# Kernel tuning notes

Measured on AMD Instinct MI355X. Metric: run time of the kernel, lower is better.

Reference implementation:

```python
import jax, jax.numpy as jnp
import numpy as np

TEMP = 0.1
EPS = 1e-08

def _l2norm(x):
    # F.normalize semantics: x / max(||x||, 1e-12)
    n = jnp.linalg.norm(x, axis=-1, keepdims=True)
    return x / jnp.maximum(n, 1e-12)

def setup_inputs() -> dict:
    key = jax.random.key(0)
    k0, k1, k2, k3, k4 = jax.random.split(key, 5)
    B, Ph, Pw, D, O = 32, 32, 32, 512, 128
    P = Ph * Pw
    patch_features = jax.random.normal(k0, (B, Ph, Pw, D), jnp.float32)
    obj_features = jax.random.normal(k1, (B, O, D), jnp.float32)
    # e1i: each patch positively matched to one object (one-hot rows)
    idx = jax.random.randint(k2, (B, P), 0, O)
    e1i = jax.nn.one_hot(idx, O, dtype=jnp.float32)
    # e1j / e2j: sparse binary negative masks
    e1j = (jax.random.uniform(k3, (B, P, P)) < 0.1).astype(jnp.float32)
    e2j = (jax.random.uniform(k4, (B, P, O)) < 0.1).astype(jnp.float32)
    return {"patch_features": patch_features, "obj_features": obj_features,
            "e1i": e1i, "e1j": e1j, "e2j": e2j}

def reference(patch_features, obj_features, e1i, e1j, e2j):
    B, D = patch_features.shape[0], patch_features.shape[-1]
    pf = patch_features.reshape(B, -1, D)          # [B, P, D]
    pn = _l2norm(pf)
    on = _l2norm(obj_features)                     # [B, O, D]
    po_sim = jnp.einsum('bpd,bod->bpo', pn, on)    # patch-object cosine sim
    po_exp = jnp.exp(po_sim / TEMP)
    pp_exp = jnp.exp(jnp.einsum('bpd,bqd->bpq', pn, pn) / TEMP)
    delta_E1i_E2i = jnp.sum(e1i * po_exp, axis=-1)     # [B, P]
    sum_E1i_E1j = jnp.sum(e1j * pp_exp, axis=-1)
    sum_E1i_E2j = jnp.sum(e2j * po_exp, axis=-1)
    ratio = delta_E1i_E2i / (delta_E1i_E2i + sum_E1i_E1j + sum_E1i_E2j + EPS)
    loss_all = -jnp.log(ratio + EPS)                   # [B, P]
    valid = (jnp.sum(e1i, axis=-1) > 0).astype(loss_all.dtype)  # [B, P]
    n_valid = jnp.sum(valid)
    loss = jnp.sum(loss_all * valid) / n_valid
    matched = jnp.argmax(po_sim, axis=-1)              # [B, P]
    labels = jnp.take_along_axis(e1i, matched[..., None], axis=-1)[..., 0]
    matched_success_ratio = jnp.sum(labels * valid) / n_valid
    return loss, matched_success_ratio
```

## Files before the change

kernel.cpp:

```cpp
#include <hip/hip_runtime.h>
#include <hip/hip_bf16.h>

constexpr int BB = 32;
constexpr int P  = 1024;
constexpr int O  = 128;
constexpr int D  = 512;
constexpr float EPS = 1e-8f;
constexpr float SCL = 14.426950408889634f;

typedef __attribute__((ext_vector_type(8))) short short8;
typedef __attribute__((ext_vector_type(16))) float f32x16;

__device__ __forceinline__ unsigned short f2bf(float f) {
  __hip_bfloat16 h = __float2bfloat16(f);
  unsigned short u;
  __builtin_memcpy(&u, &h, sizeof(u));
  return u;
}

__device__ __forceinline__ void gld_lds16(const void* g, void* l) {
  __builtin_amdgcn_global_load_lds(
      (const __attribute__((address_space(1))) void*)g,
      (__attribute__((address_space(3))) void*)l, 16, 0, 0);
}

__global__ __launch_bounds__(256) void prep_kernel(
    const float* __restrict__ pf, const float* __restrict__ of,
    __hip_bfloat16* __restrict__ pn, __hip_bfloat16* __restrict__ on) {
  int lane = threadIdx.x & 63;
  int row = blockIdx.x * 4 + (threadIdx.x >> 6);
  const float* src;
  __hip_bfloat16* dst;
  if (row < BB * P) {
    src = pf + (size_t)row * D;
    dst = pn + (size_t)row * D;
  } else {
    int r = row - BB * P;
    if (r >= BB * O) return;
    src = of + (size_t)r * D;
    dst = on + (size_t)r * D;
  }
  float4 v0 = *(const float4*)(src + lane * 8);
  float4 v1 = *(const float4*)(src + lane * 8 + 4);
  float ss = v0.x * v0.x + v0.y * v0.y + v0.z * v0.z + v0.w * v0.w +
             v1.x * v1.x + v1.y * v1.y + v1.z * v1.z + v1.w * v1.w;
  #pragma unroll
  for (int s = 1; s < 64; s <<= 1) ss += __shfl_xor(ss, s);
  float sc = 1.0f / fmaxf(sqrtf(ss), 1e-12f);
  short8 w;
  w[0] = (short)f2bf(v0.x * sc); w[1] = (short)f2bf(v0.y * sc);
  w[2] = (short)f2bf(v0.z * sc); w[3] = (short)f2bf(v0.w * sc);
  w[4] = (short)f2bf(v1.x * sc); w[5] = (short)f2bf(v1.y * sc);
  w[6] = (short)f2bf(v1.z * sc); w[7] = (short)f2bf(v1.w * sc);
  *reinterpret_cast<short8*>(dst + lane * 8) = w;
}

__global__ __launch_bounds__(256, 3) void icl_main7(
    const __hip_bfloat16* __restrict__ pn, const __hip_bfloat16* __restrict__ on,
    const float* __restrict__ e1i, const float* __restrict__ e1j,
    const float* __restrict__ e2j,
    float* __restrict__ d_row, float* __restrict__ s1_row,
    float* __restrict__ s2_row, unsigned long long* __restrict__ pk_row,
    int* __restrict__ ip_row) {

  __shared__ __hip_bfloat16 As[128 * 64];
  __shared__ __hip_bfloat16 Bs[128 * 64];

  const int tid  = threadIdx.x;
  const int l    = tid & 63;
  const int wid  = tid >> 6;
  const int wr   = wid >> 1;
  const int wc   = wid & 1;
  const int half = l >> 5;
  const int l31  = l & 31;

  const int bid   = blockIdx.x;
  const int batch = bid & 31;
  const int unit  = bid >> 5;
  const int rt    = unit & 7;
  const int ct    = unit >> 3;
  const int row0  = rt * 128;

  const __hip_bfloat16* pnb = pn + (size_t)batch * P * D;
  const __hip_bfloat16* onb = on + (size_t)batch * O * D;
  const __hip_bfloat16* asrc = pnb + (size_t)row0 * D;
  const __hip_bfloat16* bsrc = (ct == 0) ? onb : pnb + (size_t)(ct - 1) * 128 * D;

  auto stage = [&](const __hip_bfloat16* __restrict__ src,
                   __hip_bfloat16* __restrict__ lds, int k0) {
    #pragma unroll
    for (int i = 0; i < 4; ++i) {
      int q = i * 256 + tid;
      int rr = q >> 3, c = q & 7;
      int gc = c ^ (rr & 7);
      gld_lds16(src + (size_t)rr * D + k0 + (gc << 3),
                (char*)lds + (size_t)(i * 256 + wid * 64) * 16);
    }
  };

  f32x16 acc[2][2];
  #pragma unroll
  for (int m = 0; m < 2; ++m)
    #pragma unroll
    for (int n = 0; n < 2; ++n)
      #pragma unroll
      for (int k = 0; k < 16; ++k) acc[m][n][k] = 0.f;

  for (int ks = 0; ks < 8; ++ks) {
    __syncthreads();
    stage(asrc, As, ks * 64);
    stage(bsrc, Bs, ks * 64);
    __syncthreads();
    #pragma unroll
    for (int kc = 0; kc < 4; ++kc) {
      const int ch = (kc << 1) | half;
      short8 af[2], bfr[2];
      #pragma unroll
      for (int m = 0; m < 2; ++m) {
        int row = wr * 64 + m * 32 + l31;
        af[m] = *reinterpret_cast<const short8*>(
            As + row * 64 + ((ch ^ (row & 7)) << 3));
      }
      #pragma unroll
      for (int n = 0; n < 2; ++n) {
        int col = wc * 64 + n * 32 + l31;
        bfr[n] = *reinterpret_cast<const short8*>(
            Bs + col * 64 + ((ch ^ (col & 7)) << 3));
      }
      #pragma unroll
      for (int m = 0; m < 2; ++m)
        #pragma unroll
        for (int n = 0; n < 2; ++n)
          acc[m][n] = __builtin_amdgcn_mfma_f32_32x32x16_bf16(
              af[m], bfr[n], acc[m][n], 0, 0, 0);
    }
  }

  if (ct == 0) {
    #pragma unroll
    for (int m = 0; m < 2; ++m) {
      #pragma unroll
      for (int r = 0; r < 16; ++r) {
        const int lrow = wr * 64 + m * 32 + (r & 3) + ((r >> 2) << 3) + (half << 2);
        const size_t grow = (size_t)batch * P + row0 + lrow;
        const size_t gb = grow * O;
        const int c0 = wc * 64 + l31, c1 = wc * 64 + 32 + l31;
        float s0 = acc[m][0][r], s1v = acc[m][1][r];
        float e0 = exp2f(s0 * SCL), e1 = exp2f(s1v * SCL);
        float m10 = e1i[gb + c0], m11 = e1i[gb + c1];
        float m20 = e2j[gb + c0], m21 = e2j[gb + c1];
        float dv  = m10 * e0 + m11 * e1;
        float s2v = m20 * e0 + m21 * e1;
        int ipv = (m11 > 0.5f) ? c1 : ((m10 > 0.5f) ? c0 : -1);
        float mvv; int miv;
        if (s1v > s0) { mvv = s1v; miv = c1; } else { mvv = s0; miv = c0; }
        #pragma unroll
        for (int s = 1; s < 32; s <<= 1) {
          dv  += __shfl_xor(dv, s);
          s2v += __shfl_xor(s2v, s);
          ipv  = max(ipv, __shfl_xor(ipv, s));
          float ov = __shfl_xor(mvv, s);
          int   oi = __shfl_xor(miv, s);
          if (ov > mvv || (ov == mvv && oi < miv)) { mvv = ov; miv = oi; }
        }
        if (l31 == 0) {
          if (dv != 0.f) atomicAdd(&d_row[grow], dv);
          atomicAdd(&s2_row[grow], s2v);
          unsigned long long pkv =
              ((unsigned long long)__float_as_uint(mvv + 2.0f) << 32) |
              (unsigned)(0xFFFFFFFFu - (unsigned)miv);
          atomicMax(&pk_row[grow], pkv);
          if (ipv >= 0) atomicMax(&ip_row[grow], ipv);
        }
      }
    }
  } else {
    const int pb = (ct - 1) * 128;
    #pragma unroll
    for (int m = 0; m < 2; ++m) {
      #pragma unroll
      for (int r = 0; r < 16; ++r) {
        const int lrow = wr * 64 + m * 32 + (r & 3) + ((r >> 2) << 3) + (half << 2);
        const size_t grow = (size_t)batch * P + row0 + lrow;
        const size_t gb = grow * P + pb;
        const int c0 = wc * 64 + l31, c1 = wc * 64 + 32 + l31;
        float v = e1j[gb + c0] * exp2f(acc[m][0][r] * SCL) +
                  e1j[gb + c1] * exp2f(acc[m][1][r] * SCL);
        #pragma unroll
        for (int s = 1; s < 32; s <<= 1) v += __shfl_xor(v, s);
        if (l31 == 0) atomicAdd(&s1_row[grow], v);
      }
    }
  }
}

__global__ __launch_bounds__(256) void icl_reduce(
    const float* __restrict__ d_row, const float* __restrict__ s1_row,
    const float* __restrict__ s2_row, const unsigned long long* __restrict__ pk_row,
    const int* __restrict__ ip_row, float* __restrict__ accum) {
  __shared__ float red[12];
  const int tid = threadIdx.x;
  const int row = blockIdx.x * 256 + tid;
  float d = d_row[row], a = s1_row[row], c = s2_row[row];
  int ipv = ip_row[row];
  int miv = (int)(0xFFFFFFFFu - (unsigned)(pk_row[row] & 0xFFFFFFFFull));
  float valid = (ipv >= 0) ? 1.f : 0.f;
  float ratio = d / (d + a + c + EPS);
  float lsum = -logf(ratio + EPS) * valid;
  float lbl  = (ipv >= 0 && miv == ipv) ? 1.f : 0.f;
  float vct  = valid;
  #pragma unroll
  for (int s = 1; s < 64; s <<= 1) {
    lsum += __shfl_xor(lsum, s);
    lbl  += __shfl_xor(lbl, s);
    vct  += __shfl_xor(vct, s);
  }
  const int wid = tid >> 6;
  if ((tid & 63) == 0) {
    red[wid * 3 + 0] = lsum;
    red[wid * 3 + 1] = lbl;
    red[wid * 3 + 2] = vct;
  }
  __syncthreads();
  if (tid == 0) {
    atomicAdd(&accum[0], red[0] + red[3] + red[6] + red[9]);
    atomicAdd(&accum[1], red[1] + red[4] + red[7] + red[10]);
    atomicAdd(&accum[2], red[2] + red[5] + red[8] + red[11]);
  }
}

__global__ void finalize_kernel(const float* __restrict__ accum,
                                float* __restrict__ out) {
  if (threadIdx.x == 0 && blockIdx.x == 0) {
    float nv = accum[2];
    out[0] = accum[0] / nv;
    out[1] = accum[1] / nv;
  }
}

__global__ __launch_bounds__(256) void norm_kernel(
    const float* __restrict__ pf, const float* __restrict__ of,
    float* __restrict__ invp, float* __restrict__ invo) {
  int lane = threadIdx.x & 63;
  int row = blockIdx.x * 4 + (threadIdx.x >> 6);
  const float* src;
  float* dst;
  if (row < BB * P) {
    src = pf + (size_t)row * D;
    dst = invp + row;
  } else {
    int r = row - BB * P;
    if (r >= BB * O) return;
    src = of + (size_t)r * D;
    dst = invo + r;
  }
  float ss = 0.f;
  #pragma unroll
  for (int i = 0; i < 2; ++i) {
    float4 v = *(const float4*)(src + (lane + 64 * i) * 4);
    ss += v.x * v.x + v.y * v.y + v.z * v.z + v.w * v.w;
  }
  #pragma unroll
  for (int s = 1; s < 64; s <<= 1) ss += __shfl_xor(ss, s);
  if (lane == 0) *dst = 1.0f / fmaxf(sqrtf(ss), 1e-12f);
}

__global__ __launch_bounds__(256) void icl_main_v1(
    const float* __restrict__ pf, const float* __restrict__ of,
    const float* __restrict__ e1i, const float* __restrict__ e1j,
    const float* __restrict__ e2j, const float* __restrict__ invp,
    const float* __restrict__ invo, float* __restrict__ accum) {
  constexpr int PT = 128, BK = 64;
  __shared__ __hip_bfloat16 As[PT * BK];
  __shared__ __hip_bfloat16 Bs[PT * BK];
  __shared__ float d_l[2][PT], s2_l[2][PT], ei_l[2][PT], s1_l[2][PT], mv_l[2][PT];
  __shared__ int   mi_l[2][PT];
  __shared__ float red[12];

  const int tid  = threadIdx.x;
  const int lane = tid & 63;
  const int wid  = tid >> 6;
  const int wr   = wid >> 1;
  const int wc   = wid & 1;
  const int half = lane >> 5;
  const int l31  = lane & 31;
  const int b    = blockIdx.x & 31;
  const int pt   = blockIdx.x >> 5;
  const int row0 = pt * PT;

  const float* pfb = pf + (size_t)b * P * D;
  const float* ofb = of + (size_t)b * O * D;
  const float* ivp = invp + b * P + row0;
  const float* ivq = invp + b * P;
  const float* ivo = invo + b * O;

  float s1p[2][16];
  #pragma unroll
  for (int m = 0; m < 2; ++m)
    #pragma unroll
    for (int r = 0; r < 16; ++r) s1p[m][r] = 0.f;

  auto stage = [&](const float* __restrict__ src, const float* __restrict__ inv,
                   __hip_bfloat16* __restrict__ lds, int k0) {
    #pragma unroll
    for (int i = 0; i < 8; ++i) {
      int c = i * 256 + tid;
      int rr = c >> 4, kc = c & 15;
      float4 v = *(const float4*)(src + (size_t)rr * D + k0 + (kc << 2));
      float s = inv[rr];
      int off = rr * BK + ((((kc >> 1) ^ (rr & 7)) << 3) | ((kc & 1) << 2));
      ushort4 w;
      w.x = f2bf(v.x * s);
      w.y = f2bf(v.y * s);
      w.z = f2bf(v.z * s);
      w.w = f2bf(v.w * s);
      *reinterpret_cast<ushort4*>(lds + off) = w;
    }
  };

  for (int ct = 0; ct < 9; ++ct) {
    const float* bsrc = (ct == 0) ? ofb : pfb + (size_t)(ct - 1) * 128 * D;
    const float* binv = (ct == 0) ? ivo : ivq + (ct - 1) * 128;

    f32x16 acc[2][2];
    #pragma unroll
    for (int m = 0; m < 2; ++m)
      #pragma unroll
      for (int n = 0; n < 2; ++n)
        #pragma unroll
        for (int k = 0; k < 16; ++k) acc[m][n][k] = 0.f;

    for (int ks = 0; ks < D / BK; ++ks) {
      __syncthreads();
      stage(pfb + (size_t)row0 * D, ivp, As, ks * BK);
      stage(bsrc, binv, Bs, ks * BK);
      __syncthreads();
      #pragma unroll
      for (int kc = 0; kc < 4; ++kc) {
        short8 af[2], bfr[2];
        #pragma unroll
        for (int m = 0; m < 2; ++m) {
          int row = wr * 64 + m * 32 + l31;
          af[m] = *reinterpret_cast<const short8*>(
              As + row * BK + ((((kc << 1) | half) ^ (row & 7)) << 3));
        }
        #pragma unroll
        for (int n = 0; n < 2; ++n) {
          int col = wc * 64 + n * 32 + l31;
          bfr[n] = *reinterpret_cast<const short8*>(
              Bs + col * BK + ((((kc << 1) | half) ^ (col & 7)) << 3));
        }
        #pragma unroll
        for (int m = 0; m < 2; ++m)
          #pragma unroll
          for (int n = 0; n < 2; ++n)
            acc[m][n] = __builtin_amdgcn_mfma_f32_32x32x16_bf16(
                af[m], bfr[n], acc[m][n], 0, 0, 0);
      }
    }

    if (ct == 0) {
      #pragma unroll
      for (int m = 0; m < 2; ++m) {
        #pragma unroll
        for (int r = 0; r < 16; ++r) {
          int lrow = wr * 64 + m * 32 + (r & 3) + ((r >> 2) << 3) + (half << 2);
          size_t base = ((size_t)b * P + row0 + lrow) * O;
          float dsum = 0.f, s2s = 0.f, eis = 0.f, mval = -1e30f;
          int midx = 0;
          #pragma unroll
          for (int n = 0; n < 2; ++n) {
            int col = wc * 64 + n * 32 + l31;
            float sim = acc[m][n][r];
            float e = exp2f(sim * SCL);
            float v1 = e1i[base + col];
            float v2 = e2j[base + col];
            dsum += v1 * e;
            s2s  += v2 * e;
            eis  += v1;
            if (sim > mval) { mval = sim; midx = col; }
          }
          #pragma unroll
          for (int s = 1; s < 32; s <<= 1) {
            dsum += __shfl_xor(dsum, s);
            s2s  += __shfl_xor(s2s, s);
            eis  += __shfl_xor(eis, s);
            float ov = __shfl_xor(mval, s);
            int   oi = __shfl_xor(midx, s);
            if (ov > mval || (ov == mval && oi < midx)) { mval = ov; midx = oi; }
          }
          if (l31 == 0) {
            d_l[wc][lrow] = dsum;
            s2_l[wc][lrow] = s2s;
            ei_l[wc][lrow] = eis;
            mv_l[wc][lrow] = mval;
            mi_l[wc][lrow] = midx;
          }
        }
      }
    } else {
      const int qbase = (ct - 1) * 128;
      #pragma unroll
      for (int m = 0; m < 2; ++m) {
        #pragma unroll
        for (int r = 0; r < 16; ++r) {
          int lrow = wr * 64 + m * 32 + (r & 3) + ((r >> 2) << 3) + (half << 2);
          size_t base = ((size_t)b * P + row0 + lrow) * P + qbase;
          float s = 0.f;
          #pragma unroll
          for (int n = 0; n < 2; ++n) {
            int col = wc * 64 + n * 32 + l31;
            s += e1j[base + col] * exp2f(acc[m][n][r] * SCL);
          }
          s1p[m][r] += s;
        }
      }
    }
  }

  #pragma unroll
  for (int m = 0; m < 2; ++m) {
    #pragma unroll
    for (int r = 0; r < 16; ++r) {
      float v = s1p[m][r];
      #pragma unroll
      for (int s = 1; s < 32; s <<= 1) v += __shfl_xor(v, s);
      if (l31 == 0) {
        int lrow = wr * 64 + m * 32 + (r & 3) + ((r >> 2) << 3) + (half << 2);
        s1_l[wc][lrow] = v;
      }
    }
  }
  __syncthreads();

  float lsum = 0.f, lbl = 0.f, vct = 0.f;
  if (tid < PT) {
    float delta = d_l[0][tid] + d_l[1][tid];
    float s2 = s2_l[0][tid] + s2_l[1][tid];
    float eis = ei_l[0][tid] + ei_l[1][tid];
    float s1 = s1_l[0][tid] + s1_l[1][tid];
    float m0 = mv_l[0][tid], m1 = mv_l[1][tid];
    int mi = (m1 > m0) ? mi_l[1][tid] : mi_l[0][tid];
    float valid = (eis > 0.f) ? 1.f : 0.f;
    float ratio = delta / (delta + s1 + s2 + EPS);
    float loss = -logf(ratio + EPS);
    float label = e1i[((size_t)b * P + row0 + tid) * O + mi];
    lsum = loss * valid;
    lbl  = label * valid;
    vct  = valid;
  }
  #pragma unroll
  for (int s = 1; s < 64; s <<= 1) {
    lsum += __shfl_xor(lsum, s);
    lbl  += __shfl_xor(lbl, s);
    vct  += __shfl_xor(vct, s);
  }
  if (lane == 0) {
    red[wid * 3 + 0] = lsum;
    red[wid * 3 + 1] = lbl;
    red[wid * 3 + 2] = vct;
  }
  __syncthreads();
  if (tid == 0) {
    float a = red[0] + red[3] + red[6] + red[9];
    float c = red[1] + red[4] + red[7] + red[10];
    float v = red[2] + red[5] + red[8] + red[11];
    atomicAdd(&accum[0], a);
    atomicAdd(&accum[1], c);
    atomicAdd(&accum[2], v);
  }
}

extern "C" void kernel_launch(void* const* d_in, const int* in_sizes, int n_in,
                              void* d_out, int out_size, void* d_ws, size_t ws_size,
                              hipStream_t stream) {
  const float* pf  = (const float*)d_in[0];
  const float* of  = (const float*)d_in[1];
  const float* e1i = (const float*)d_in[2];
  const float* e1j = (const float*)d_in[3];
  const float* e2j = (const float*)d_in[4];

  char* base = (char*)d_ws;
  constexpr size_t NR = (size_t)BB * P;
  float* accum                 = (float*)base;
  float* d_row                 = (float*)(base + 64);
  float* s1_row                = (float*)(base + 64 + 4 * NR);
  float* s2_row                = (float*)(base + 64 + 8 * NR);
  unsigned long long* pk_row   = (unsigned long long*)(base + 64 + 12 * NR);
  int* ip_row                  = (int*)(base + 64 + 20 * NR);
  __hip_bfloat16* pn           = (__hip_bfloat16*)(base + 64 + 24 * NR);
  const size_t pn_bytes = (size_t)BB * P * D * 2;
  const size_t on_bytes = (size_t)BB * O * D * 2;
  __hip_bfloat16* on           = (__hip_bfloat16*)(base + 64 + 24 * NR + pn_bytes);
  const size_t need = 64 + 24 * NR + pn_bytes + on_bytes;

  if (ws_size >= need) {
    hipMemsetAsync(base, 0, 64 + 20 * NR, stream);
    hipMemsetAsync(ip_row, 0xFF, 4 * NR, stream);
    prep_kernel<<<(BB * P + BB * O) / 4, 256, 0, stream>>>(pf, of, pn, on);
    icl_main7<<<BB * 72, 256, 0, stream>>>(pn, on, e1i, e1j, e2j,
                                           d_row, s1_row, s2_row, pk_row, ip_row);
    icl_reduce<<<NR / 256, 256, 0, stream>>>(d_row, s1_row, s2_row, pk_row,
                                             ip_row, accum);
  } else {
    float* ws   = (float*)d_ws;
    float* invp = ws + 16;
    float* invo = ws + 16 + BB * P;
    hipMemsetAsync(accum, 0, 16 * sizeof(float), stream);
    norm_kernel<<<(BB * P + BB * O) / 4, 256, 0, stream>>>(pf, of, invp, invo);
    icl_main_v1<<<BB * (P / 128), 256, 0, stream>>>(pf, of, e1i, e1j, e2j,
                                                    invp, invo, accum);
  }
  finalize_kernel<<<1, 64, 0, stream>>>(accum, (float*)d_out);
}
```

Measured before the change: 151.0 us.

## Use 256x256 double-buffered tiles for patch-patch GEMM and split object blocks

The main kernel moves to 512-thread blocks. Patch-patch work now uses 256x256 output tiles per block with double-buffered LDS staging, so each block issues fewer global loads per output and overlaps the next k-slice load with MFMA work. Object-similarity tiles get a dedicated 128x128 path in which each of 8 waves owns a 64x32 slab. The larger LDS footprint (128KB) and higher accumulator register count limit occupancy, and the prefetch is issued without an explicit wait before compute, which relies on the trailing barrier for correctness.

Result: slower. 190.9 us (+26.4%).

```diff
diff --git a/kernel.cpp b/kernel.cpp
--- a/kernel.cpp
+++ b/kernel.cpp
@@ -55,7 +55,7 @@
   *reinterpret_cast<short8*>(dst + lane * 8) = w;
 }
 
-__global__ __launch_bounds__(256, 3) void icl_main7(
+__global__ __launch_bounds__(512, 2) void icl_main8(
     const __hip_bfloat16* __restrict__ pn, const __hip_bfloat16* __restrict__ on,
     const float* __restrict__ e1i, const float* __restrict__ e1j,
     const float* __restrict__ e2j,
@@ -63,80 +63,75 @@
     float* __restrict__ s2_row, unsigned long long* __restrict__ pk_row,
     int* __restrict__ ip_row) {
 
-  __shared__ __hip_bfloat16 As[128 * 64];
-  __shared__ __hip_bfloat16 Bs[128 * 64];
+  __shared__ __hip_bfloat16 As[2][256 * 64];
+  __shared__ __hip_bfloat16 Bs[2][256 * 64];
 
   const int tid  = threadIdx.x;
   const int l    = tid & 63;
   const int wid  = tid >> 6;
-  const int wr   = wid >> 1;
-  const int wc   = wid & 1;
   const int half = l >> 5;
   const int l31  = l & 31;
 
   const int bid   = blockIdx.x;
-  const int batch = bid & 31;
-  const int unit  = bid >> 5;
-  const int rt    = unit & 7;
-  const int ct    = unit >> 3;
-  const int row0  = rt * 128;
-
-  const __hip_bfloat16* pnb = pn + (size_t)batch * P * D;
-  const __hip_bfloat16* onb = on + (size_t)batch * O * D;
-  const __hip_bfloat16* asrc = pnb + (size_t)row0 * D;
-  const __hip_bfloat16* bsrc = (ct == 0) ? onb : pnb + (size_t)(ct - 1) * 128 * D;
-
-  auto stage = [&](const __hip_bfloat16* __restrict__ src,
-                   __hip_bfloat16* __restrict__ lds, int k0) {
-    #pragma unroll
-    for (int i = 0; i < 4; ++i) {
-      int q = i * 256 + tid;
-      int rr = q >> 3, c = q & 7;
-      int gc = c ^ (rr & 7);
-      gld_lds16(src + (size_t)rr * D + k0 + (gc << 3),
-                (char*)lds + (size_t)(i * 256 + wid * 64) * 16);
-    }
-  };
-
-  f32x16 acc[2][2];
-  #pragma unroll
-  for (int m = 0; m < 2; ++m)
-    #pragma unroll
-    for (int n = 0; n < 2; ++n)
-      #pragma unroll
-      for (int k = 0; k < 16; ++k) acc[m][n][k] = 0.f;
-
-  for (int ks = 0; ks < 8; ++ks) {
+  const bool isobj = bid < 256;
+
+  if (isobj) {
+    const int batch = bid & 31;
+    const int rt    = bid >> 5;
+    const int row0  = rt * 128;
+    const int wr    = wid >> 2;
+    const int wc    = wid & 3;
+
+    const __hip_bfloat16* asrc = pn + (size_t)batch * P * D + (size_t)row0 * D;
+    const __hip_bfloat16* bsrc = on + (size_t)batch * O * D;
+
+    f32x16 acc[2];
+    #pragma unroll
+    for (int m = 0; m < 2; ++m)
+      #pragma unroll
+      for (int k = 0; k < 16; ++k) acc[m][k] = 0.f;
+
+    auto stage = [&](const __hip_bfloat16* src, __hip_bfloat16* lds, int k0) {
+      #pragma unroll
+      for (int i = 0; i < 2; ++i) {
+        int q = i * 512 + tid;
+        int rr = q >> 3, c = q & 7;
+        int gc = c ^ (rr & 7);
+        gld_lds16(src + (size_t)rr * D + k0 + (gc << 3),
+                  (char*)lds + (size_t)(i * 512 + wid * 64) * 16);
+      }
+    };
+
+    stage(asrc, &As[0][0], 0);
+    stage(bsrc, &Bs[0][0], 0);
     __syncthreads();
-    stage(asrc, As, ks * 64);
-    stage(bsrc, Bs, ks * 64);
-    __syncthreads();
-    #pragma unroll
-    for (int kc = 0; kc < 4; ++kc) {
-      const int ch = (kc << 1) | half;
-      short8 af[2], bfr[2];
-      #pragma unroll
-      for (int m = 0; m < 2; ++m) {
-        int row = wr * 64 + m * 32 + l31;
-        af[m] = *reinterpret_cast<const short8*>(
-            As + row * 64 + ((ch ^ (row & 7)) << 3));
-      }
-      #pragma unroll
-      for (int n = 0; n < 2; ++n) {
-        int col = wc * 64 + n * 32 + l31;
-        bfr[n] = *reinterpret_cast<const short8*>(
-            Bs + col * 64 + ((ch ^ (col & 7)) << 3));
-      }
-      #pragma unroll
-      for (int m = 0; m < 2; ++m)
-        #pragma unroll
-        for (int n = 0; n < 2; ++n)
-          acc[m][n] = __builtin_amdgcn_mfma_f32_32x32x16_bf16(
-              af[m], bfr[n], acc[m][n], 0, 0, 0);
-    }
-  }
-
-  if (ct == 0) {
+    int cur = 0;
+
+    for (int ks = 0; ks < 8; ++ks) {
+      if (ks < 7) {
+        stage(asrc, &As[cur ^ 1][0], (ks + 1) * 64);
+        stage(bsrc, &Bs[cur ^ 1][0], (ks + 1) * 64);
+      }
+      const __hip_bfloat16* ab = &As[cur][0];
+      const __hip_bfloat16* bb = &Bs[cur][0];
+      #pragma unroll
+      for (int kc = 0; kc < 4; ++kc) {
+        const int ch = (kc << 1) | half;
+        const int bcol = wc * 32 + l31;
+        short8 bf = *reinterpret_cast<const short8*>(
+            bb + bcol * 64 + ((ch ^ (bcol & 7)) << 3));
+        #pragma unroll
+        for (int m = 0; m < 2; ++m) {
+          int arow = wr * 64 + m * 32 + l31;
+          short8 af = *reinterpret_cast<const short8*>(
+              ab + arow * 64 + ((ch ^ (arow & 7)) << 3));
+          acc[m] = __builtin_amdgcn_mfma_f32_32x32x16_bf16(af, bf, acc[m], 0, 0, 0);
+        }
+      }
+      __syncthreads();
+      cur ^= 1;
+    }
+
     #pragma unroll
     for (int m = 0; m < 2; ++m) {
       #pragma unroll
@@ -144,16 +139,16 @@
         const int lrow = wr * 64 + m * 32 + (r & 3) + ((r >> 2) << 3) + (half << 2);
         const size_t grow = (size_t)batch * P + row0 + lrow;
         const size_t gb = grow * O;
-        const int c0 = wc * 64 + l31, c1 = wc * 64 + 32 + l31;
-        float s0 = acc[m][0][r], s1v = acc[m][1][r];
-        float e0 = exp2f(s0 * SCL), e1 = exp2f(s1v * SCL);
-        float m10 = e1i[gb + c0], m11 = e1i[gb + c1];
-        float m20 = e2j[gb + c0], m21 = e2j[gb + c1];
-        float dv  = m10 * e0 + m11 * e1;
-        float s2v = m20 * e0 + m21 * e1;
-        int ipv = (m11 > 0.5f) ? c1 : ((m10 > 0.5f) ? c0 : -1);
-        float mvv; int miv;
-        if (s1v > s0) { mvv = s1v; miv = c1; } else { mvv = s0; miv = c0; }
+        const int c0 = wc * 32 + l31;
+        float sim = acc[m][r];
+        float e = exp2f(sim * SCL);
+        float m1 = e1i[gb + c0];
+        float m2 = e2j[gb + c0];
+        float dv  = m1 * e;
+        float s2v = m2 * e;
+        int   ipv = (m1 > 0.5f) ? c0 : -1;
+        float mvv = sim;
+        int   miv = c0;
         #pragma unroll
         for (int s = 1; s < 32; s <<= 1) {
           dv  += __shfl_xor(dv, s);
@@ -175,17 +170,85 @@
       }
     }
   } else {
-    const int pb = (ct - 1) * 128;
-    #pragma unroll
-    for (int m = 0; m < 2; ++m) {
+    const int pid   = bid - 256;
+    const int batch = pid & 31;
+    const int u     = pid >> 5;
+    const int rt    = u & 3;
+    const int ct    = u >> 2;
+    const int row0  = rt * 256;
+    const int pb    = ct * 256;
+    const int wr    = wid >> 2;
+    const int wcg   = wid & 3;
+
+    const __hip_bfloat16* pnb  = pn + (size_t)batch * P * D;
+    const __hip_bfloat16* asrc = pnb + (size_t)row0 * D;
+    const __hip_bfloat16* bsrc = pnb + (size_t)pb * D;
+
+    f32x16 acc[4][2];
+    #pragma unroll
+    for (int m = 0; m < 4; ++m)
+      #pragma unroll
+      for (int n = 0; n < 2; ++n)
+        #pragma unroll
+        for (int k = 0; k < 16; ++k) acc[m][n][k] = 0.f;
+
+    auto stage = [&](const __hip_bfloat16* src, __hip_bfloat16* lds, int k0) {
+      #pragma unroll
+      for (int i = 0; i < 4; ++i) {
+        int q = i * 512 + tid;
+        int rr = q >> 3, c = q & 7;
+        int gc = c ^ (rr & 7);
+        gld_lds16(src + (size_t)rr * D + k0 + (gc << 3),
+                  (char*)lds + (size_t)(i * 512 + wid * 64) * 16);
+      }
+    };
+
+    stage(asrc, &As[0][0], 0);
+    stage(bsrc, &Bs[0][0], 0);
+    __syncthreads();
+    int cur = 0;
+
+    for (int ks = 0; ks < 8; ++ks) {
+      if (ks < 7) {
+        stage(asrc, &As[cur ^ 1][0], (ks + 1) * 64);
+        stage(bsrc, &Bs[cur ^ 1][0], (ks + 1) * 64);
+      }
+      const __hip_bfloat16* ab = &As[cur][0];
+      const __hip_bfloat16* bb = &Bs[cur][0];
+      #pragma unroll
+      for (int kc = 0; kc < 4; ++kc) {
+        const int ch = (kc << 1) | half;
+        short8 bf[2];
+        #pragma unroll
+        for (int n = 0; n < 2; ++n) {
+          int bcol = wcg * 64 + n * 32 + l31;
+          bf[n] = *reinterpret_cast<const short8*>(
+              bb + bcol * 64 + ((ch ^ (bcol & 7)) << 3));
+        }
+        #pragma unroll
+        for (int m = 0; m < 4; ++m) {
+          int arow = wr * 128 + m * 32 + l31;
+          short8 af = *reinterpret_cast<const short8*>(
+              ab + arow * 64 + ((ch ^ (arow & 7)) << 3));
+          #pragma unroll
+          for (int n = 0; n < 2; ++n)
+            acc[m][n] = __builtin_amdgcn_mfma_f32_32x32x16_bf16(
+                af, bf[n], acc[m][n], 0, 0, 0);
+        }
+      }
+      __syncthreads();
+      cur ^= 1;
+    }
+
+    #pragma unroll
+    for (int m = 0; m < 4; ++m) {
       #pragma unroll
       for (int r = 0; r < 16; ++r) {
-        const int lrow = wr * 64 + m * 32 + (r & 3) + ((r >> 2) << 3) + (half << 2);
+        const int lrow = wr * 128 + m * 32 + (r & 3) + ((r >> 2) << 3) + (half << 2);
         const size_t grow = (size_t)batch * P + row0 + lrow;
-        const size_t gb = grow * P + pb;
-        const int c0 = wc * 64 + l31, c1 = wc * 64 + 32 + l31;
-        float v = e1j[gb + c0] * exp2f(acc[m][0][r] * SCL) +
-                  e1j[gb + c1] * exp2f(acc[m][1][r] * SCL);
+        const size_t gb = grow * P + pb + wcg * 64;
+        float v = e1j[gb + l31] * exp2f(acc[m][0][r] * SCL) +
+                  e1j[gb + 32 + l31] * exp2f(acc[m][1][r] * SCL);
         #pragma unroll
         for (int s = 1; s < 32; s <<= 1) v += __shfl_xor(v, s);
         if (l31 == 0) atomicAdd(&s1_row[grow], v);
@@ -498,8 +561,8 @@
     hipMemsetAsync(base, 0, 64 + 20 * NR, stream);
     hipMemsetAsync(ip_row, 0xFF, 4 * NR, stream);
     prep_kernel<<<(BB * P + BB * O) / 4, 256, 0, stream>>>(pf, of, pn, on);
-    icl_main7<<<BB * 72, 256, 0, stream>>>(pn, on, e1i, e1j, e2j,
-                                           d_row, s1_row, s2_row, pk_row, ip_row);
+    icl_main8<<<768, 512, 0, stream>>>(pn, on, e1i, e1j, e2j,
+                                       d_row, s1_row, s2_row, pk_row, ip_row);
     icl_reduce<<<NR / 256, 256, 0, stream>>>(d_row, s1_row, s2_row, pk_row,
                                              ip_row, accum);
   } else {
```

## Double-buffer LDS tiles in main GEMM kernel to overlap loads with MFMA

Applied to the files above, without the earlier changes.

Adds a second LDS buffer for the A and B tiles and prefetches the next K-slice with global_load_lds while MFMAs run on the current slice. Explicit vmcnt waits and s_barrier calls replace the two __syncthreads per iteration. LDS use doubles to 64KB per block and the launch bound drops from 3 to 2 blocks per CU, trading occupancy for latency hiding.

New measurement: 197.9 us. 1.31x slower.

```diff
diff --git a/kernel.cpp b/kernel.cpp
--- a/kernel.cpp
+++ b/kernel.cpp
@@ -55,7 +55,7 @@
   *reinterpret_cast<short8*>(dst + lane * 8) = w;
 }
 
-__global__ __launch_bounds__(256, 3) void icl_main7(
+__global__ __launch_bounds__(256, 2) void icl_main9(
     const __hip_bfloat16* __restrict__ pn, const __hip_bfloat16* __restrict__ on,
     const float* __restrict__ e1i, const float* __restrict__ e1j,
     const float* __restrict__ e2j,
@@ -63,8 +63,8 @@
     float* __restrict__ s2_row, unsigned long long* __restrict__ pk_row,
     int* __restrict__ ip_row) {
 
-  __shared__ __hip_bfloat16 As[128 * 64];
-  __shared__ __hip_bfloat16 Bs[128 * 64];
+  __shared__ __hip_bfloat16 As[2][128 * 64];
+  __shared__ __hip_bfloat16 Bs[2][128 * 64];
 
   const int tid  = threadIdx.x;
   const int l    = tid & 63;
@@ -106,11 +106,23 @@
       #pragma unroll
       for (int k = 0; k < 16; ++k) acc[m][n][k] = 0.f;
 
+  stage(asrc, &As[0][0], 0);
+  stage(bsrc, &Bs[0][0], 0);
+  int cur = 0;
+
   for (int ks = 0; ks < 8; ++ks) {
-    __syncthreads();
-    stage(asrc, As, ks * 64);
-    stage(bsrc, Bs, ks * 64);
-    __syncthreads();
+    if (ks < 7) {
+      stage(asrc, &As[cur ^ 1][0], (ks + 1) * 64);
+      stage(bsrc, &Bs[cur ^ 1][0], (ks + 1) * 64);
+      asm volatile("s_waitcnt vmcnt(8)" ::: "memory");
+    } else {
+      asm volatile("s_waitcnt vmcnt(0)" ::: "memory");
+    }
+    __builtin_amdgcn_s_barrier();
+    __builtin_amdgcn_sched_barrier(0);
+
+    const __hip_bfloat16* ab = &As[cur][0];
+    const __hip_bfloat16* bb = &Bs[cur][0];
     #pragma unroll
     for (int kc = 0; kc < 4; ++kc) {
       const int ch = (kc << 1) | half;
@@ -119,13 +131,13 @@
       for (int m = 0; m < 2; ++m) {
         int row = wr * 64 + m * 32 + l31;
         af[m] = *reinterpret_cast<const short8*>(
-            As + row * 64 + ((ch ^ (row & 7)) << 3));
+            ab + row * 64 + ((ch ^ (row & 7)) << 3));
       }
       #pragma unroll
       for (int n = 0; n < 2; ++n) {
         int col = wc * 64 + n * 32 + l31;
         bfr[n] = *reinterpret_cast<const short8*>(
-            Bs + col * 64 + ((ch ^ (col & 7)) << 3));
+            bb + col * 64 + ((ch ^ (col & 7)) << 3));
       }
       #pragma unroll
       for (int m = 0; m < 2; ++m)
@@ -134,6 +146,10 @@
           acc[m][n] = __builtin_amdgcn_mfma_f32_32x32x16_bf16(
               af[m], bfr[n], acc[m][n], 0, 0, 0);
     }
+
+    __builtin_amdgcn_sched_barrier(0);
+    __builtin_amdgcn_s_barrier();
+    cur ^= 1;
   }
 
   if (ct == 0) {
@@ -498,7 +514,7 @@
     hipMemsetAsync(base, 0, 64 + 20 * NR, stream);
     hipMemsetAsync(ip_row, 0xFF, 4 * NR, stream);
     prep_kernel<<<(BB * P + BB * O) / 4, 256, 0, stream>>>(pf, of, pn, on);
-    icl_main7<<<BB * 72, 256, 0, stream>>>(pn, on, e1i, e1j, e2j,
+    icl_main9<<<BB * 72, 256, 0, stream>>>(pn, on, e1i, e1j, e2j,
                                            d_row, s1_row, s2_row, pk_row, ip_row);
     icl_reduce<<<NR / 256, 256, 0, stream>>>(d_row, s1_row, s2_row, pk_row,
                                              ip_row, accum);
```

## Pre-pack dense float masks into bitmasks in prep kernel before GEMM epilogue

Applied to the files above, without the earlier changes.

The prep kernel now also streams e1j, e2j and e1i and packs them with wave ballots: bitmasks for e1j and e2j, and the index of the first positive object per row for e1i. The main GEMM epilogue then loads one 64-bit word per row instead of many strided float loads, and drops the ip_row atomic and its memset. The aim is to move the large mask traffic into a fully coalesced streaming pass and lighten the epilogue. The cost is an extra bitmask write and re-read, plus a larger workspace. It also assumes e1i rows are one-hot when computing the positive term.

Result: slower. 176.6 us (+16.9%).

```diff
diff --git a/kernel.cpp b/kernel.cpp
--- a/kernel.cpp
+++ b/kernel.cpp
@@ -24,44 +24,74 @@
       (__attribute__((address_space(3))) void*)l, 16, 0, 0);
 }
 
-__global__ __launch_bounds__(256) void prep_kernel(
+constexpr int FB = (BB * P + BB * O) / 4;
+constexpr int JB = (BB * P) / 4;
+__global__ __launch_bounds__(256) void prep2_kernel(
     const float* __restrict__ pf, const float* __restrict__ of,
-    __hip_bfloat16* __restrict__ pn, __hip_bfloat16* __restrict__ on) {
-  int lane = threadIdx.x & 63;
-  int row = blockIdx.x * 4 + (threadIdx.x >> 6);
-  const float* src;
-  __hip_bfloat16* dst;
-  if (row < BB * P) {
-    src = pf + (size_t)row * D;
-    dst = pn + (size_t)row * D;
-  } else {
-    int r = row - BB * P;
-    if (r >= BB * O) return;
-    src = of + (size_t)r * D;
-    dst = on + (size_t)r * D;
-  }
-  float4 v0 = *(const float4*)(src + lane * 8);
-  float4 v1 = *(const float4*)(src + lane * 8 + 4);
-  float ss = v0.x * v0.x + v0.y * v0.y + v0.z * v0.z + v0.w * v0.w +
-             v1.x * v1.x + v1.y * v1.y + v1.z * v1.z + v1.w * v1.w;
-  #pragma unroll
-  for (int s = 1; s < 64; s <<= 1) ss += __shfl_xor(ss, s);
-  float sc = 1.0f / fmaxf(sqrtf(ss), 1e-12f);
-  short8 w;
-  w[0] = (short)f2bf(v0.x * sc); w[1] = (short)f2bf(v0.y * sc);
-  w[2] = (short)f2bf(v0.z * sc); w[3] = (short)f2bf(v0.w * sc);
-  w[4] = (short)f2bf(v1.x * sc); w[5] = (short)f2bf(v1.y * sc);
-  w[6] = (short)f2bf(v1.z * sc); w[7] = (short)f2bf(v1.w * sc);
-  *reinterpret_cast<short8*>(dst + lane * 8) = w;
-}
-
-__global__ __launch_bounds__(256, 3) void icl_main7(
-    const __hip_bfloat16* __restrict__ pn, const __hip_bfloat16* __restrict__ on,
     const float* __restrict__ e1i, const float* __restrict__ e1j,
     const float* __restrict__ e2j,
+    __hip_bfloat16* __restrict__ pn, __hip_bfloat16* __restrict__ on,
+    unsigned long long* __restrict__ bm1j, unsigned long long* __restrict__ bm2j,
+    int* __restrict__ posr) {
+  const int lane = threadIdx.x & 63;
+  const int wid4 = threadIdx.x >> 6;
+  const int bid  = blockIdx.x;
+
+  if (bid < FB) {
+    int row = bid * 4 + wid4;
+    const float* src;
+    __hip_bfloat16* dst;
+    if (row < BB * P) {
+      src = pf + (size_t)row * D;
+      dst = pn + (size_t)row * D;
+    } else {
+      int r = row - BB * P;
+      if (r >= BB * O) return;
+      src = of + (size_t)r * D;
+      dst = on + (size_t)r * D;
+    }
+    float4 v0 = *(const float4*)(src + lane * 8);
+    float4 v1 = *(const float4*)(src + lane * 8 + 4);
+    float ss = v0.x * v0.x + v0.y * v0.y + v0.z * v0.z + v0.w * v0.w +
+               v1.x * v1.x + v1.y * v1.y + v1.z * v1.z + v1.w * v1.w;
+    #pragma unroll
+    for (int s = 1; s < 64; s <<= 1) ss += __shfl_xor(ss, s);
+    float sc = 1.0f / fmaxf(sqrtf(ss), 1e-12f);
+    short8 w;
+    w[0] = (short)f2bf(v0.x * sc); w[1] = (short)f2bf(v0.y * sc);
+    w[2] = (short)f2bf(v0.z * sc); w[3] = (short)f2bf(v0.w * sc);
+    w[4] = (short)f2bf(v1.x * sc); w[5] = (short)f2bf(v1.y * sc);
+    w[6] = (short)f2bf(v1.z * sc); w[7] = (short)f2bf(v1.w * sc);
+    *reinterpret_cast<short8*>(dst + lane * 8) = w;
+  } else if (bid < FB + JB) {
+    const int row = (bid - FB) * 4 + wid4;
+    const float* src = e1j + (size_t)row * P;
+    #pragma unroll
+    for (int it = 0; it < 16; ++it) {
+      unsigned long long b = __ballot(src[it * 64 + lane] > 0.5f);
+      if (lane == 0) bm1j[(size_t)row * 16 + it] = b;
+    }
+  } else {
+    const int row = (bid - FB - JB) * 4 + wid4;
+    unsigned long long b0 = __ballot(e1i[(size_t)row * O + lane] > 0.5f);
+    unsigned long long b1 = __ballot(e1i[(size_t)row * O + 64 + lane] > 0.5f);
+    unsigned long long d0 = __ballot(e2j[(size_t)row * O + lane] > 0.5f);
+    unsigned long long d1 = __ballot(e2j[(size_t)row * O + 64 + lane] > 0.5f);
+    if (lane == 0) {
+      posr[row] = b0 ? (__ffsll(b0) - 1) : (b1 ? 63 + __ffsll(b1) : -1);
+      bm2j[(size_t)row * 2]     = d0;
+      bm2j[(size_t)row * 2 + 1] = d1;
+    }
+  }
+}
+
+__global__ __launch_bounds__(256, 3) void icl_main10(
+    const __hip_bfloat16* __restrict__ pn, const __hip_bfloat16* __restrict__ on,
+    const unsigned long long* __restrict__ bm1j,
+    const unsigned long long* __restrict__ bm2j,
+    const int* __restrict__ posr,
     float* __restrict__ d_row, float* __restrict__ s1_row,
-    float* __restrict__ s2_row, unsigned long long* __restrict__ pk_row,
-    int* __restrict__ ip_row) {
+    float* __restrict__ s2_row, unsigned long long* __restrict__ pk_row) {
 
   __shared__ __hip_bfloat16 As[128 * 64];
   __shared__ __hip_bfloat16 Bs[128 * 64];
@@ -143,22 +173,20 @@
       for (int r = 0; r < 16; ++r) {
         const int lrow = wr * 64 + m * 32 + (r & 3) + ((r >> 2) << 3) + (half << 2);
         const size_t grow = (size_t)batch * P + row0 + lrow;
-        const size_t gb = grow * O;
-        const int c0 = wc * 64 + l31, c1 = wc * 64 + 32 + l31;
+        const int pos = posr[grow];
+        const unsigned long long W2 = bm2j[grow * 2 + wc];
+        const int c0 = wc * 64 + l31, c1 = c0 + 32;
         float s0 = acc[m][0][r], s1v = acc[m][1][r];
-        float e0 = exp2f(s0 * SCL), e1 = exp2f(s1v * SCL);
-        float m10 = e1i[gb + c0], m11 = e1i[gb + c1];
-        float m20 = e2j[gb + c0], m21 = e2j[gb + c1];
-        float dv  = m10 * e0 + m11 * e1;
-        float s2v = m20 * e0 + m21 * e1;
-        int ipv = (m11 > 0.5f) ? c1 : ((m10 > 0.5f) ? c0 : -1);
+        float e0 = exp2f(s0 * SCL), e1v = exp2f(s1v * SCL);
+        float dv  = (c0 == pos ? e0 : 0.f) + (c1 == pos ? e1v : 0.f);
+        float s2v = (((W2 >> l31) & 1) ? e0 : 0.f) +
+                    (((W2 >> (32 + l31)) & 1) ? e1v : 0.f);
         float mvv; int miv;
         if (s1v > s0) { mvv = s1v; miv = c1; } else { mvv = s0; miv = c0; }
         #pragma unroll
         for (int s = 1; s < 32; s <<= 1) {
           dv  += __shfl_xor(dv, s);
           s2v += __shfl_xor(s2v, s);
-          ipv  = max(ipv, __shfl_xor(ipv, s));
           float ov = __shfl_xor(mvv, s);
           int   oi = __shfl_xor(miv, s);
           if (ov > mvv || (ov == mvv && oi < miv)) { mvv = ov; miv = oi; }
@@ -170,44 +198,42 @@
               ((unsigned long long)__float_as_uint(mvv + 2.0f) << 32) |
               (unsigned)(0xFFFFFFFFu - (unsigned)miv);
           atomicMax(&pk_row[grow], pkv);
-          if (ipv >= 0) atomicMax(&ip_row[grow], ipv);
         }
       }
     }
   } else {
-    const int pb = (ct - 1) * 128;
+    const int widx = (ct - 1) * 2 + wc;
     #pragma unroll
     for (int m = 0; m < 2; ++m) {
       #pragma unroll
       for (int r = 0; r < 16; ++r) {
         const int lrow = wr * 64 + m * 32 + (r & 3) + ((r >> 2) << 3) + (half << 2);
         const size_t grow = (size_t)batch * P + row0 + lrow;
-        const size_t gb = grow * P + pb;
-        const int c0 = wc * 64 + l31, c1 = wc * 64 + 32 + l31;
-        float v = e1j[gb + c0] * exp2f(acc[m][0][r] * SCL) +
-                  e1j[gb + c1] * exp2f(acc[m][1][r] * SCL);
+        const unsigned long long W = bm1j[grow * 16 + widx];
+        float v = (((W >> l31) & 1) ? exp2f(acc[m][0][r] * SCL) : 0.f) +
+                  (((W >> (32 + l31)) & 1) ? exp2f(acc[m][1][r] * SCL) : 0.f);
         #pragma unroll
         for (int s = 1; s < 32; s <<= 1) v += __shfl_xor(v, s);
-        if (l31 == 0) atomicAdd(&s1_row[grow], v);
-      }
-    }
-  }
-}
-
-__global__ __launch_bounds__(256) void icl_reduce(
+        if (l31 == 0 && v != 0.f) atomicAdd(&s1_row[grow], v);
+      }
+    }
+  }
+}
+
+__global__ __launch_bounds__(256) void icl_reduce2(
     const float* __restrict__ d_row, const float* __restrict__ s1_row,
     const float* __restrict__ s2_row, const unsigned long long* __restrict__ pk_row,
-    const int* __restrict__ ip_row, float* __restrict__ accum) {
+    const int* __restrict__ posr, float* __restrict__ accum) {
   __shared__ float red[12];
   const int tid = threadIdx.x;
   const int row = blockIdx.x * 256 + tid;
   float d = d_row[row], a = s1_row[row], c = s2_row[row];
-  int ipv = ip_row[row];
+  int pos = posr[row];
   int miv = (int)(0xFFFFFFFFu - (unsigned)(pk_row[row] & 0xFFFFFFFFull));
-  float valid = (ipv >= 0) ? 1.f : 0.f;
+  float valid = (pos >= 0) ? 1.f : 0.f;
   float ratio = d / (d + a + c + EPS);
   float lsum = -logf(ratio + EPS) * valid;
-  float lbl  = (ipv >= 0 && miv == ipv) ? 1.f : 0.f;
+  float lbl  = (pos >= 0 && miv == pos) ? 1.f : 0.f;
   float vct  = valid;
   #pragma unroll
   for (int s = 1; s < 64; s <<= 1) {
@@ -482,26 +508,28 @@
 
   char* base = (char*)d_ws;
   constexpr size_t NR = (size_t)BB * P;
-  float* accum                 = (float*)base;
-  float* d_row                 = (float*)(base + 64);
-  float* s1_row                = (float*)(base + 64 + 4 * NR);
-  float* s2_row                = (float*)(base + 64 + 8 * NR);
-  unsigned long long* pk_row   = (unsigned long long*)(base + 64 + 12 * NR);
-  int* ip_row                  = (int*)(base + 64 + 20 * NR);
-  __hip_bfloat16* pn           = (__hip_bfloat16*)(base + 64 + 24 * NR);
+  float* accum               = (float*)base;
+  float* d_row               = (float*)(base + 64);
+  float* s1_row              = (float*)(base + 64 + 4 * NR);
+  float* s2_row              = (float*)(base + 64 + 8 * NR);
+  unsigned long long* pk_row = (unsigned long long*)(base + 64 + 12 * NR);
+  unsigned long long* bm1j   = (unsigned long long*)(base + 64 + 20 * NR);
+  unsigned long long* bm2j   = (unsigned long long*)(base + 64 + 148 * NR);
+  int* posr                  = (int*)(base + 64 + 164 * NR);
+  __hip_bfloat16* pn         = (__hip_bfloat16*)(base + 64 + 168 * NR);
   const size_t pn_bytes = (size_t)BB * P * D * 2;
   const size_t on_bytes = (size_t)BB * O * D * 2;
-  __hip_bfloat16* on           = (__hip_bfloat16*)(base + 64 + 24 * NR + pn_bytes);
-  const size_t need = 64 + 24 * NR + pn_bytes + on_bytes;
+  __hip_bfloat16* on         = (__hip_bfloat16*)(base + 64 + 168 * NR + pn_bytes);
+  const size_t need = 64 + 168 * NR + pn_bytes + on_bytes;
 
   if (ws_size >= need) {
     hipMemsetAsync(base, 0, 64 + 20 * NR, stream);
-    hipMemsetAsync(ip_row, 0xFF, 4 * NR, stream);
-    prep_kernel<<<(BB * P + BB * O) / 4, 256, 0, stream>>>(pf, of, pn, on);
-    icl_main7<<<BB * 72, 256, 0, stream>>>(pn, on, e1i, e1j, e2j,
-                                           d_row, s1_row, s2_row, pk_row, ip_row);
-    icl_reduce<<<NR / 256, 256, 0, stream>>>(d_row, s1_row, s2_row, pk_row,
-                                             ip_row, accum);
+    prep2_kernel<<<FB + 2 * JB, 256, 0, stream>>>(pf, of, e1i, e1j, e2j,
+                                                  pn, on, bm1j, bm2j, posr);
+    icl_main10<<<BB * 72, 256, 0, stream>>>(pn, on, bm1j, bm2j, posr,
+                                            d_row, s1_row, s2_row, pk_row);
+    icl_reduce2<<<NR / 256, 256, 0, stream>>>(d_row, s1_row, s2_row, pk_row,
+                                              posr, accum);
   } else {
     float* ws   = (float*)d_ws;
     float* invp = ws + 16;
```
